# Optimization experiments

Measured on AMD Instinct MI355X. Metric: run time of the kernel, lower is better.

## Reference

```python
import jax, jax.numpy as jnp
import numpy as np

B, T, D, R = 4, 2048, 1024, 32


def setup_inputs() -> dict:
    key = jax.random.key(0)
    kx, ku = jax.random.split(key)
    x = jax.random.normal(kx, (B, T, D), dtype=jnp.float32)
    # low-rank metric factor; small init so distances are moderate
    U = jax.random.normal(ku, (D, R), dtype=jnp.float32) * 0.05
    return {"x": x, "U": U}


def reference(x, U):
    # g = U @ U.T (PSD low-rank metric).
    # dist_sq[b,t,j] = (x_t - x_j)^T g (x_t - x_j)
    #               = ||U^T x_t||^2 + ||U^T x_j||^2 - 2 (U^T x_t).(U^T x_j)
    # Algebraic expansion of the original O(B*T*T*D) broadcasted diff tensor.
    y = jnp.einsum('btd,dr->btr', x, U)                # [B,T,R]
    n = jnp.sum(y * y, axis=-1)                         # [B,T]
    cross = jnp.einsum('btr,bjr->btj', y, y)            # [B,T,T]
    dist_sq = n[:, :, None] + n[:, None, :] - 2.0 * cross
    attn = jax.nn.softmax(-dist_sq, axis=-1)            # [B,T,T]
    return jnp.einsum('btj,bjd->btd', attn, x)          # [B,T,D]
```

## Files before the change

### kernel.cpp

```cpp
#include <hip/hip_runtime.h>

#define B_ 4
#define T_ 2048
#define D_ 1024
#define R_ 32
#define XSTR2 136

typedef __attribute__((ext_vector_type(8))) short short8;
typedef __attribute__((ext_vector_type(4))) float f32x4;
typedef __attribute__((ext_vector_type(4))) unsigned short us4;
typedef __attribute__((ext_vector_type(8))) unsigned short us8;

__device__ __forceinline__ unsigned short f2bf(float f) {
  union { float f; unsigned u; } v; v.f = f;
  unsigned r = (v.u + 0x7fffu + ((v.u >> 16) & 1u)) >> 16;
  return (unsigned short)r;
}
__device__ __forceinline__ float bf2f(unsigned short h) {
  union { unsigned u; float f; } v; v.u = (unsigned)h << 16;
  return v.f;
}

__global__ __launch_bounds__(256)
void geo_ut(const float* __restrict__ U, unsigned short* __restrict__ Ut) {
  __shared__ float tile[128][33];
  const int tid = threadIdx.x;
  const int d0 = blockIdx.x * 128;
  #pragma unroll
  for (int i = 0; i < 16; i++) {
    int e = i * 256 + tid;
    int d = e >> 5, r = e & 31;
    tile[d][r] = U[(size_t)(d0 + d) * R_ + r];
  }
  __syncthreads();
  const int r = tid >> 3, seg = tid & 7;
  us8 o0, o1;
  #pragma unroll
  for (int k = 0; k < 8; k++) o0[k] = f2bf(tile[seg * 16 + k][r]);
  #pragma unroll
  for (int k = 0; k < 8; k++) o1[k] = f2bf(tile[seg * 16 + 8 + k][r]);
  *(us8*)(Ut + (size_t)r * D_ + d0 + seg * 16) = o0;
  *(us8*)(Ut + (size_t)r * D_ + d0 + seg * 16 + 8) = o1;
}

__global__ __launch_bounds__(256)
void geo_prep(const float* __restrict__ x, const unsigned short* __restrict__ Ut,
              unsigned short* __restrict__ xt, float* __restrict__ y_part) {
  __shared__ unsigned short xs[2][32 * XSTR2];
  const int b = blockIdx.y, slab = blockIdx.z;
  const int t0 = blockIdx.x * 32;
  const int d0 = slab * 256;
  const int tid = threadIdx.x, w = tid >> 6, lane = tid & 63;
  const int m = lane & 15, quad = lane >> 4;
  const int Mt = w & 1, Nt = w >> 1;
  const int lr = tid >> 3;
  const int lc = (tid & 7) * 16;

  const float* xb = x + ((size_t)b * T_ + t0 + lr) * D_ + d0 + lc;
  float4 v[2][4];
  #pragma unroll
  for (int ch = 0; ch < 2; ch++)
    #pragma unroll
    for (int i = 0; i < 4; i++)
      v[ch][i] = *(const float4*)(xb + ch * 128 + i * 4);
  #pragma unroll
  for (int ch = 0; ch < 2; ch++)
    #pragma unroll
    for (int i = 0; i < 4; i++) {
      us4 c;
      c[0] = f2bf(v[ch][i].x); c[1] = f2bf(v[ch][i].y);
      c[2] = f2bf(v[ch][i].z); c[3] = f2bf(v[ch][i].w);
      *(us4*)&xs[ch][lr * XSTR2 + lc + i * 4] = c;
    }
  __syncthreads();
  {
    const int wd = tid >> 1, wt = (tid & 1) * 16;
    #pragma unroll
    for (int ch = 0; ch < 2; ch++) {
      us8 o0, o1;
      #pragma unroll
      for (int k = 0; k < 8; k++) {
        o0[k] = xs[ch][(wt + k) * XSTR2 + wd];
        o1[k] = xs[ch][(wt + 8 + k) * XSTR2 + wd];
      }
      unsigned short* xo = xt + ((size_t)b * D_ + d0 + ch * 128 + wd) * T_ + t0;
      *(us8*)(xo + wt) = o0;
      *(us8*)(xo + wt + 8) = o1;
    }
  }
  f32x4 acc = {0.f, 0.f, 0.f, 0.f};
  #pragma unroll
  for (int ch = 0; ch < 2; ch++)
    #pragma unroll
    for (int ks = 0; ks < 4; ks++) {
      short8 af = *(const short8*)&xs[ch][(Mt * 16 + m) * XSTR2 + ks * 32 + quad * 8];
      short8 bf = *(const short8*)(Ut + (size_t)(Nt * 16 + m) * D_ + d0 + ch * 128 + ks * 32 + quad * 8);
      acc = __builtin_amdgcn_mfma_f32_16x16x32_bf16(af, bf, acc, 0, 0, 0);
    }
  float* yp = y_part + ((size_t)(slab * B_ + b) * T_ + t0 + Mt * 16 + quad * 4) * R_ + Nt * 16 + m;
  #pragma unroll
  for (int k = 0; k < 4; k++) yp[(size_t)k * R_] = acc[k];
}

__global__ __launch_bounds__(256)
void geo_reduce(const float* __restrict__ y_part, unsigned short* __restrict__ ybf,
                float* __restrict__ nsq, float* __restrict__ l) {
  const int tid = threadIdx.x;
  const size_t row = (size_t)blockIdx.x * 32 + (tid >> 3);
  const int r0 = (tid & 7) * 4;
  f32x4 v = {0.f, 0.f, 0.f, 0.f};
  #pragma unroll
  for (int s = 0; s < 4; s++) {
    f32x4 p = *(const f32x4*)(y_part + ((size_t)s * B_ * T_ + row) * R_ + r0);
    #pragma unroll
    for (int k = 0; k < 4; k++) v[k] += p[k];
  }
  us4 pk;
  float part = 0.f;
  #pragma unroll
  for (int k = 0; k < 4; k++) {
    pk[k] = f2bf(1.41421356237f * v[k]);
    float b = bf2f(pk[k]);
    part += b * b;
  }
  *(us4*)(ybf + row * R_ + r0) = pk;
  part += __shfl_xor(part, 1, 64);
  part += __shfl_xor(part, 2, 64);
  part += __shfl_xor(part, 4, 64);
  if ((tid & 7) == 0) { nsq[row] = 0.5f * part; l[row] = 0.f; }
}

__global__ __launch_bounds__(256)
void geo_scores(const unsigned short* __restrict__ ybf,
                const float* __restrict__ nsq,
                unsigned short* __restrict__ P, float* __restrict__ l,
                int jg0, int Kslab) {
  const int b = blockIdx.z;
  const int t0 = blockIdx.x * 128;
  const int jl0 = blockIdx.y * 128;
  const int tid = threadIdx.x, w = tid >> 6, lane = tid & 63;
  const int m = lane & 15, quad = lane >> 4;
  const unsigned short* yb = ybf + (size_t)b * T_ * R_;
  const float* nb = nsq + b * T_;
  const int jw = jl0 + w * 32;
  short8 aj[2]; f32x4 njv[2];
  #pragma unroll
  for (int rb = 0; rb < 2; rb++) {
    aj[rb] = *(const short8*)(yb + (size_t)(jg0 + jw + rb * 16 + m) * R_ + quad * 8);
    njv[rb] = *(const f32x4*)(nb + jg0 + jw + rb * 16 + quad * 4);
  }
  unsigned short* Pb = P + (size_t)b * T_ * Kslab;
  short8 btn = *(const short8*)(yb + (size_t)(t0 + m) * R_ + quad * 8);
  float ntn = nb[t0 + m];
  #pragma unroll 2
  for (int cb = 0; cb < 8; cb++) {
    const int t = t0 + cb * 16 + m;
    short8 bt = btn;
    float nt = ntn;
    if (cb < 7) {
      btn = *(const short8*)(yb + (size_t)(t + 16) * R_ + quad * 8);
      ntn = nb[t + 16];
    }
    float ls = 0.f;
    #pragma unroll
    for (int rb = 0; rb < 2; rb++) {
      f32x4 z = {0.f, 0.f, 0.f, 0.f};
      f32x4 c = __builtin_amdgcn_mfma_f32_16x16x32_bf16(aj[rb], bt, z, 0, 0, 0);
      us4 pk;
      #pragma unroll
      for (int r = 0; r < 4; r++) {
        float p = __expf(c[r] - njv[rb][r] - nt);
        ls += p;
        pk[r] = f2bf(p);
      }
      *(us4*)(Pb + (size_t)t * Kslab + jw + rb * 16 + quad * 4) = pk;
    }
    ls += __shfl_xor(ls, 16, 64);
    ls += __shfl_xor(ls, 32, 64);
    if (quad == 0) atomicAdd(&l[b * T_ + t], ls);
  }
}

__global__ __launch_bounds__(256)
void geo_pv(const unsigned short* __restrict__ P,
            const unsigned short* __restrict__ xt,
            const float* __restrict__ l, float* __restrict__ out,
            int Kslab, int kxt0, int accumulate, int normalize) {
  __shared__ unsigned short As[128 * 64];
  __shared__ unsigned short Bs[128 * 64];
  const int b = blockIdx.z;
  const int id = blockIdx.x;
  const int cls = id & 7, kk = id >> 3;
  const int t0 = (2 * cls + (kk >> 3)) * 128;
  const int d0 = (kk & 7) * 128;
  const int tid = threadIdx.x, w = tid >> 6, lane = tid & 63;
  const int m = lane & 15, quad = lane >> 4;
  const int wr = (w & 1) * 64, wc = (w >> 1) * 64;
  const int srow = lane >> 3, sslot = lane & 7;
  const unsigned short* Pb = P + ((size_t)b * T_ + t0) * Kslab;
  const unsigned short* Xb = xt + ((size_t)b * D_ + d0) * T_ + kxt0;
  f32x4 acc[4][4];
  #pragma unroll
  for (int i = 0; i < 4; i++)
    #pragma unroll
    for (int j = 0; j < 4; j++) acc[i][j] = (f32x4){0.f, 0.f, 0.f, 0.f};

  for (int k0 = 0; k0 < Kslab; k0 += 64) {
    __syncthreads();
    #pragma unroll
    for (int cc = 0; cc < 4; cc++) {
      const int row = w * 32 + cc * 8 + srow;
      const int gs = sslot ^ (row & 7);
      __builtin_amdgcn_global_load_lds(
          (const __attribute__((address_space(1))) void*)(Pb + (size_t)row * Kslab + k0 + gs * 8),
          (__attribute__((address_space(3))) void*)(As + (w * 32 + cc * 8) * 64),
          16, 0, 0);
      __builtin_amdgcn_global_load_lds(
          (const __attribute__((address_space(1))) void*)(Xb + (size_t)row * T_ + k0 + gs * 8),
          (__attribute__((address_space(3))) void*)(Bs + (w * 32 + cc * 8) * 64),
          16, 0, 0);
    }
    __syncthreads();
    #pragma unroll
    for (int ks = 0; ks < 2; ks++) {
      short8 af[4], bf[4];
      #pragma unroll
      for (int i = 0; i < 4; i++) {
        const int ra = wr + i * 16 + m;
        af[i] = *(const short8*)(As + ra * 64 + (((ks * 4 + quad) ^ (m & 7)) * 8));
        const int cd = wc + i * 16 + m;
        bf[i] = *(const short8*)(Bs + cd * 64 + (((ks * 4 + quad) ^ (m & 7)) * 8));
      }
      #pragma unroll
      for (int rb = 0; rb < 4; rb++)
        #pragma unroll
        for (int cb = 0; cb < 4; cb++)
          acc[rb][cb] = __builtin_amdgcn_mfma_f32_16x16x32_bf16(af[rb], bf[cb], acc[rb][cb], 0, 0, 0);
    }
  }
  float* ob = out + ((size_t)b * T_ + t0 + wr) * D_ + d0 + wc;
  #pragma unroll
  for (int rb = 0; rb < 4; rb++) {
    f32x4 lv = *(const f32x4*)(l + b * T_ + t0 + wr + rb * 16 + quad * 4);
    f32x4 inv;
    #pragma unroll
    for (int r = 0; r < 4; r++) inv[r] = 1.f / lv[r];
    #pragma unroll
    for (int cb = 0; cb < 4; cb++) {
      #pragma unroll
      for (int r = 0; r < 4; r++) {
        float* p = ob + (size_t)(rb * 16 + quad * 4 + r) * D_ + cb * 16 + m;
        float v = acc[rb][cb][r];
        if (accumulate) v += *p;
        if (normalize) v *= inv[r];
        *p = v;
      }
    }
  }
}

extern "C" void kernel_launch(void* const* d_in, const int* in_sizes, int n_in,
                              void* d_out, int out_size, void* d_ws, size_t ws_size,
                              hipStream_t stream) {
  const float* x = (const float*)d_in[0];
  const float* U = (const float*)d_in[1];
  float* out = (float*)d_out;

  const size_t xt_b  = (size_t)B_ * D_ * T_ * 2;
  const size_t ybf_b = (size_t)B_ * T_ * R_ * 2;
  const size_t nsq_b = (size_t)B_ * T_ * 4;
  const size_t l_b   = nsq_b;
  const size_t ut_b  = (size_t)D_ * R_ * 2;
  const size_t yp_b  = (size_t)4 * B_ * T_ * R_ * 4;
  const size_t base  = xt_b + ybf_b + nsq_b + l_b + ut_b + yp_b;
  const size_t pfull = (size_t)B_ * T_ * T_ * 2;

  int nslab = 16;
  const int cand[5] = {1, 2, 4, 8, 16};
  for (int i = 0; i < 5; i++)
    if (base + pfull / (size_t)cand[i] <= ws_size) { nslab = cand[i]; break; }
  const int Kslab = T_ / nslab;

  char* wp = (char*)d_ws;
  unsigned short* xtp = (unsigned short*)wp;                 wp += xt_b;
  unsigned short* ybf = (unsigned short*)wp;                 wp += ybf_b;
  float* nsq = (float*)wp;                                   wp += nsq_b;
  float* lp  = (float*)wp;                                   wp += l_b;
  unsigned short* Utp = (unsigned short*)wp;                 wp += ut_b;
  float* ypart = (float*)wp;                                 wp += yp_b;
  unsigned short* P = (unsigned short*)wp;

  hipLaunchKernelGGL(geo_ut, dim3(D_ / 128), dim3(256), 0, stream, U, Utp);
  hipLaunchKernelGGL(geo_prep, dim3(T_ / 32, B_, 4), dim3(256), 0, stream,
                     x, Utp, xtp, ypart);
  hipLaunchKernelGGL(geo_reduce, dim3(B_ * T_ / 32), dim3(256), 0, stream,
                     ypart, ybf, nsq, lp);
  for (int s = 0; s < nslab; s++) {
    hipLaunchKernelGGL(geo_scores, dim3(T_ / 128, Kslab / 128, B_), dim3(256), 0, stream,
                       ybf, nsq, P, lp, s * Kslab, Kslab);
    hipLaunchKernelGGL(geo_pv, dim3(128, 1, B_), dim3(256), 0, stream,
                       P, xtp, lp, out, Kslab, s * Kslab,
                       (int)(s > 0), (int)(s == nslab - 1));
  }
}
```

Measured before the change: 155.6 us.

## Fuse score computation and PV product into one flash-style kernel

```diff
diff --git a/kernel.cpp b/kernel.cpp
--- a/kernel.cpp
+++ b/kernel.cpp
@@ -5,6 +5,10 @@
 #define D_ 1024
 #define R_ 32
 #define XSTR2 136
+#define TT 64
+#define TD 128
+#define TJ 64
+#define PSTR 72
 
 typedef __attribute__((ext_vector_type(8))) short short8;
 typedef __attribute__((ext_vector_type(4))) float f32x4;
@@ -104,7 +108,7 @@
 
 __global__ __launch_bounds__(256)
 void geo_reduce(const float* __restrict__ y_part, unsigned short* __restrict__ ybf,
-                float* __restrict__ nsq, float* __restrict__ l) {
+                float* __restrict__ nsq) {
   const int tid = threadIdx.x;
   const size_t row = (size_t)blockIdx.x * 32 + (tid >> 3);
   const int r0 = (tid & 7) * 4;
@@ -127,135 +131,122 @@
   part += __shfl_xor(part, 1, 64);
   part += __shfl_xor(part, 2, 64);
   part += __shfl_xor(part, 4, 64);
-  if ((tid & 7) == 0) { nsq[row] = 0.5f * part; l[row] = 0.f; }
-}
-
-__global__ __launch_bounds__(256)
-void geo_scores(const unsigned short* __restrict__ ybf,
-                const float* __restrict__ nsq,
-                unsigned short* __restrict__ P, float* __restrict__ l,
-                int jg0, int Kslab) {
+  if ((tid & 7) == 0) nsq[row] = 0.5f * part;
+}
+
+__global__ __launch_bounds__(256)
+void geo_fused(const unsigned short* __restrict__ ybf,
+               const float* __restrict__ nsq,
+               const unsigned short* __restrict__ xt,
+               float* __restrict__ out) {
+  __shared__ unsigned short XtS[TD * TJ];
+  __shared__ unsigned short Pbuf[TT * PSTR];
+  __shared__ float lred[4][TT];
   const int b = blockIdx.z;
-  const int t0 = blockIdx.x * 128;
-  const int jl0 = blockIdx.y * 128;
+  const int dt = blockIdx.x & 7, tt = blockIdx.x >> 3;
+  const int t0 = tt * TT, d0 = dt * TD;
   const int tid = threadIdx.x, w = tid >> 6, lane = tid & 63;
   const int m = lane & 15, quad = lane >> 4;
+  const int srow = lane >> 3, sslot = lane & 7;
   const unsigned short* yb = ybf + (size_t)b * T_ * R_;
-  const float* nb = nsq + b * T_;
-  const int jw = jl0 + w * 32;
-  short8 aj[2]; f32x4 njv[2];
-  #pragma unroll
-  for (int rb = 0; rb < 2; rb++) {
-    aj[rb] = *(const short8*)(yb + (size_t)(jg0 + jw + rb * 16 + m) * R_ + quad * 8);
-    njv[rb] = *(const f32x4*)(nb + jg0 + jw + rb * 16 + quad * 4);
-  }
-  unsigned short* Pb = P + (size_t)b * T_ * Kslab;
-  short8 btn = *(const short8*)(yb + (size_t)(t0 + m) * R_ + quad * 8);
-  float ntn = nb[t0 + m];
-  #pragma unroll 2
-  for (int cb = 0; cb < 8; cb++) {
-    const int t = t0 + cb * 16 + m;
-    short8 bt = btn;
-    float nt = ntn;
-    if (cb < 7) {
-      btn = *(const short8*)(yb + (size_t)(t + 16) * R_ + quad * 8);
-      ntn = nb[t + 16];
-    }
-    float ls = 0.f;
-    #pragma unroll
-    for (int rb = 0; rb < 2; rb++) {
+  const float* nb = nsq + (size_t)b * T_;
+  const unsigned short* xtb = xt + ((size_t)b * D_ + d0) * T_;
+
+  short8 aq[4]; f32x4 ntv[4];
+  #pragma unroll
+  for (int s = 0; s < 4; s++) {
+    aq[s]  = *(const short8*)(yb + (size_t)(t0 + s * 16 + m) * R_ + quad * 8);
+    ntv[s] = *(const f32x4*)(nb + t0 + s * 16 + quad * 4);
+  }
+  f32x4 acc[4][2];
+  f32x4 lsum[4];
+  #pragma unroll
+  for (int s = 0; s < 4; s++) {
+    lsum[s] = (f32x4){0.f, 0.f, 0.f, 0.f};
+    acc[s][0] = (f32x4){0.f, 0.f, 0.f, 0.f};
+    acc[s][1] = (f32x4){0.f, 0.f, 0.f, 0.f};
+  }
+
+  for (int j0 = 0; j0 < T_; j0 += TJ) {
+    if (j0) __syncthreads();
+    #pragma unroll
+    for (int cc = 0; cc < 4; cc++) {
+      const int rd = w * 32 + cc * 8 + srow;
+      const int gs = sslot ^ (rd & 7);
+      __builtin_amdgcn_global_load_lds(
+          (const __attribute__((address_space(1))) void*)(xtb + (size_t)rd * T_ + j0 + gs * 8),
+          (__attribute__((address_space(3))) void*)(XtS + (w * 32 + cc * 8) * 64),
+          16, 0, 0);
+    }
+    short8 bj = *(const short8*)(yb + (size_t)(j0 + w * 16 + m) * R_ + quad * 8);
+    float nj = nb[j0 + w * 16 + m];
+    #pragma unroll
+    for (int s = 0; s < 4; s++) {
       f32x4 z = {0.f, 0.f, 0.f, 0.f};
-      f32x4 c = __builtin_amdgcn_mfma_f32_16x16x32_bf16(aj[rb], bt, z, 0, 0, 0);
-      us4 pk;
+      f32x4 c = __builtin_amdgcn_mfma_f32_16x16x32_bf16(aq[s], bj, z, 0, 0, 0);
       #pragma unroll
       for (int r = 0; r < 4; r++) {
-        float p = __expf(c[r] - njv[rb][r] - nt);
-        ls += p;
-        pk[r] = f2bf(p);
+        float p = __expf(c[r] - nj - ntv[s][r]);
+        lsum[s][r] += p;
+        Pbuf[(s * 16 + quad * 4 + r) * PSTR + w * 16 + m] = f2bf(p);
       }
-      *(us4*)(Pb + (size_t)t * Kslab + jw + rb * 16 + quad * 4) = pk;
-    }
-    ls += __shfl_xor(ls, 16, 64);
-    ls += __shfl_xor(ls, 32, 64);
-    if (quad == 0) atomicAdd(&l[b * T_ + t], ls);
-  }
-}
-
-__global__ __launch_bounds__(256)
-void geo_pv(const unsigned short* __restrict__ P,
-            const unsigned short* __restrict__ xt,
-            const float* __restrict__ l, float* __restrict__ out,
-            int Kslab, int kxt0, int accumulate, int normalize) {
-  __shared__ unsigned short As[128 * 64];
-  __shared__ unsigned short Bs[128 * 64];
-  const int b = blockIdx.z;
-  const int id = blockIdx.x;
-  const int cls = id & 7, kk = id >> 3;
-  const int t0 = (2 * cls + (kk >> 3)) * 128;
-  const int d0 = (kk & 7) * 128;
-  const int tid = threadIdx.x, w = tid >> 6, lane = tid & 63;
-  const int m = lane & 15, quad = lane >> 4;
-  const int wr = (w & 1) * 64, wc = (w >> 1) * 64;
-  const int srow = lane >> 3, sslot = lane & 7;
-  const unsigned short* Pb = P + ((size_t)b * T_ + t0) * Kslab;
-  const unsigned short* Xb = xt + ((size_t)b * D_ + d0) * T_ + kxt0;
-  f32x4 acc[4][4];
-  #pragma unroll
-  for (int i = 0; i < 4; i++)
-    #pragma unroll
-    for (int j = 0; j < 4; j++) acc[i][j] = (f32x4){0.f, 0.f, 0.f, 0.f};
-
-  for (int k0 = 0; k0 < Kslab; k0 += 64) {
+    }
     __syncthreads();
-    #pragma unroll
-    for (int cc = 0; cc < 4; cc++) {
-      const int row = w * 32 + cc * 8 + srow;
-      const int gs = sslot ^ (row & 7);
-      __builtin_amdgcn_global_load_lds(
-          (const __attribute__((address_space(1))) void*)(Pb + (size_t)row * Kslab + k0 + gs * 8),
-          (__attribute__((address_space(3))) void*)(As + (w * 32 + cc * 8) * 64),
-          16, 0, 0);
-      __builtin_amdgcn_global_load_lds(
-          (const __attribute__((address_space(1))) void*)(Xb + (size_t)row * T_ + k0 + gs * 8),
-          (__attribute__((address_space(3))) void*)(Bs + (w * 32 + cc * 8) * 64),
-          16, 0, 0);
-    }
-    __syncthreads();
-    #pragma unroll
-    for (int ks = 0; ks < 2; ks++) {
-      short8 af[4], bf[4];
-      #pragma unroll
-      for (int i = 0; i < 4; i++) {
-        const int ra = wr + i * 16 + m;
-        af[i] = *(const short8*)(As + ra * 64 + (((ks * 4 + quad) ^ (m & 7)) * 8));
-        const int cd = wc + i * 16 + m;
-        bf[i] = *(const short8*)(Bs + cd * 64 + (((ks * 4 + quad) ^ (m & 7)) * 8));
+    short8 bx[2][2];
+    #pragma unroll
+    for (int nt = 0; nt < 2; nt++) {
+      const int dloc = w * 32 + nt * 16 + m;
+      #pragma unroll
+      for (int ks = 0; ks < 2; ks++)
+        bx[nt][ks] = *(const short8*)(XtS + dloc * 64 + (((ks * 4 + quad) ^ (m & 7)) * 8));
+    }
+    #pragma unroll
+    for (int s = 0; s < 4; s++) {
+      short8 a0 = *(const short8*)(Pbuf + (s * 16 + m) * PSTR + quad * 8);
+      short8 a1 = *(const short8*)(Pbuf + (s * 16 + m) * PSTR + 32 + quad * 8);
+      #pragma unroll
+      for (int nt = 0; nt < 2; nt++) {
+        acc[s][nt] = __builtin_amdgcn_mfma_f32_16x16x32_bf16(a0, bx[nt][0], acc[s][nt], 0, 0, 0);
+        acc[s][nt] = __builtin_amdgcn_mfma_f32_16x16x32_bf16(a1, bx[nt][1], acc[s][nt], 0, 0, 0);
       }
-      #pragma unroll
-      for (int rb = 0; rb < 4; rb++)
-        #pragma unroll
-        for (int cb = 0; cb < 4; cb++)
-          acc[rb][cb] = __builtin_amdgcn_mfma_f32_16x16x32_bf16(af[rb], bf[cb], acc[rb][cb], 0, 0, 0);
-    }
-  }
-  float* ob = out + ((size_t)b * T_ + t0 + wr) * D_ + d0 + wc;
-  #pragma unroll
-  for (int rb = 0; rb < 4; rb++) {
-    f32x4 lv = *(const f32x4*)(l + b * T_ + t0 + wr + rb * 16 + quad * 4);
+    }
+  }
+  #pragma unroll
+  for (int s = 0; s < 4; s++)
+    #pragma unroll
+    for (int r = 0; r < 4; r++) {
+      float v = lsum[s][r];
+      v += __shfl_xor(v, 1, 64);
+      v += __shfl_xor(v, 2, 64);
+      v += __shfl_xor(v, 4, 64);
+      v += __shfl_xor(v, 8, 64);
+      lsum[s][r] = v;
+    }
+  if (m == 0) {
+    #pragma unroll
+    for (int s = 0; s < 4; s++)
+      *(f32x4*)&lred[w][s * 16 + quad * 4] = lsum[s];
+  }
+  __syncthreads();
+  float* ob = out + ((size_t)b * T_ + t0) * D_ + d0;
+  #pragma unroll
+  for (int s = 0; s < 4; s++) {
+    f32x4 lt = *(const f32x4*)&lred[0][s * 16 + quad * 4];
+    #pragma unroll
+    for (int ww = 1; ww < 4; ww++) {
+      f32x4 lv = *(const f32x4*)&lred[ww][s * 16 + quad * 4];
+      #pragma unroll
+      for (int r = 0; r < 4; r++) lt[r] += lv[r];
+    }
     f32x4 inv;
     #pragma unroll
-    for (int r = 0; r < 4; r++) inv[r] = 1.f / lv[r];
-    #pragma unroll
-    for (int cb = 0; cb < 4; cb++) {
-      #pragma unroll
-      for (int r = 0; r < 4; r++) {
-        float* p = ob + (size_t)(rb * 16 + quad * 4 + r) * D_ + cb * 16 + m;
-        float v = acc[rb][cb][r];
-        if (accumulate) v += *p;
-        if (normalize) v *= inv[r];
-        *p = v;
-      }
-    }
+    for (int r = 0; r < 4; r++) inv[r] = 1.f / lt[r];
+    #pragma unroll
+    for (int nt = 0; nt < 2; nt++)
+      #pragma unroll
+      for (int r = 0; r < 4; r++)
+        ob[(size_t)(s * 16 + quad * 4 + r) * D_ + w * 32 + nt * 16 + m] =
+            acc[s][nt][r] * inv[r];
   }
 }
 
@@ -269,37 +260,22 @@
   const size_t xt_b  = (size_t)B_ * D_ * T_ * 2;
   const size_t ybf_b = (size_t)B_ * T_ * R_ * 2;
   const size_t nsq_b = (size_t)B_ * T_ * 4;
-  const size_t l_b   = nsq_b;
   const size_t ut_b  = (size_t)D_ * R_ * 2;
   const size_t yp_b  = (size_t)4 * B_ * T_ * R_ * 4;
-  const size_t base  = xt_b + ybf_b + nsq_b + l_b + ut_b + yp_b;
-  const size_t pfull = (size_t)B_ * T_ * T_ * 2;
-
-  int nslab = 16;
-  const int cand[5] = {1, 2, 4, 8, 16};
-  for (int i = 0; i < 5; i++)
-    if (base + pfull / (size_t)cand[i] <= ws_size) { nslab = cand[i]; break; }
-  const int Kslab = T_ / nslab;
 
   char* wp = (char*)d_ws;
-  unsigned short* xtp = (unsigned short*)wp;                 wp += xt_b;
-  unsigned short* ybf = (unsigned short*)wp;                 wp += ybf_b;
-  float* nsq = (float*)wp;                                   wp += nsq_b;
-  float* lp  = (float*)wp;                                   wp += l_b;
-  unsigned short* Utp = (unsigned short*)wp;                 wp += ut_b;
-  float* ypart = (float*)wp;                                 wp += yp_b;
-  unsigned short* P = (unsigned short*)wp;
+  unsigned short* xtp = (unsigned short*)wp;           wp += xt_b;
+  unsigned short* ybf = (unsigned short*)wp;           wp += ybf_b;
+  float* nsq = (float*)wp;                             wp += nsq_b;
+  unsigned short* Utp = (unsigned short*)wp;           wp += ut_b;
+  float* ypart = (float*)wp;                           wp += yp_b;
+  (void)ws_size;
 
   hipLaunchKernelGGL(geo_ut, dim3(D_ / 128), dim3(256), 0, stream, U, Utp);
   hipLaunchKernelGGL(geo_prep, dim3(T_ / 32, B_, 4), dim3(256), 0, stream,
                      x, Utp, xtp, ypart);
   hipLaunchKernelGGL(geo_reduce, dim3(B_ * T_ / 32), dim3(256), 0, stream,
-                     ypart, ybf, nsq, lp);
-  for (int s = 0; s < nslab; s++) {
-    hipLaunchKernelGGL(geo_scores, dim3(T_ / 128, Kslab / 128, B_), dim3(256), 0, stream,
-                       ybf, nsq, P, lp, s * Kslab, Kslab);
-    hipLaunchKernelGGL(geo_pv, dim3(128, 1, B_), dim3(256), 0, stream,
-                       P, xtp, lp, out, Kslab, s * Kslab,
-                       (int)(s > 0), (int)(s == nslab - 1));
-  }
-}
+                     ypart, ybf, nsq);
+  hipLaunchKernelGGL(geo_fused, dim3((T_ / TT) * (D_ / TD), 1, B_), dim3(256), 0, stream,
+                     ybf, nsq, xtp, out);
+}
```

New measurement: 181.8 us. +16.8%, slower.
